# Kernel tuning notes

Hardware: AMD Instinct MI355X
Metric: run time of the kernel (lower is better)

## Reference

```python
import jax, jax.numpy as jnp
import numpy as np

N = 100000   # nodes
E = 1600000  # edges
H = 8        # heads
D = 16       # per-head dim
HD = H * D   # 128 = hidden_dim * num_heads == input_dim
G = 128      # graphs in batch
OUT = 64     # output_dim
EPS = 1e-3   # BatchNorm eps
NEG_SLOPE = 0.2
THRESH = 0.5


def setup_inputs() -> dict:
    key = jax.random.key(0)
    ks = jax.random.split(key, 20)
    rn = lambda k, s: jax.random.normal(k, s, jnp.float32) * 0.1
    return {
        "h": jax.random.normal(ks[0], (N, HD), jnp.float32),
        "src": jax.random.randint(ks[1], (E,), 0, N),
        "dst": jax.random.randint(ks[2], (E,), 0, N),
        "graph_ids": jnp.sort(jax.random.randint(ks[3], (N,), 0, G)),
        # GAT layer 0 params
        "W0": rn(ks[4], (HD, HD)), "al0": rn(ks[5], (H, D)), "ar0": rn(ks[6], (H, D)), "b0": rn(ks[7], (HD,)),
        "g0": jnp.ones((HD,), jnp.float32), "be0": jnp.zeros((HD,), jnp.float32),
        # GAT layer 1 params
        "W1": rn(ks[8], (HD, HD)), "al1": rn(ks[9], (H, D)), "ar1": rn(ks[10], (H, D)), "b1": rn(ks[11], (HD,)),
        "g1": jnp.ones((HD,), jnp.float32), "be1": jnp.zeros((HD,), jnp.float32),
        # MaskLinear prediction head
        "pred_W": rn(ks[12], (OUT, HD)), "pred_b": rn(ks[13], (OUT,)),
        "mask_real": jax.random.uniform(ks[14], (OUT, HD), jnp.float32),
    }


def _gat(h, W, al, ar, b, src, dst):
    # DGL GATConv: fc -> per-node attn halves -> edge LeakyReLU -> segment softmax over dst -> scatter-add
    feat = (h @ W).reshape(N, H, D)                 # [N,H,D]
    el = jnp.sum(feat * al, axis=-1)                # [N,H]
    er = jnp.sum(feat * ar, axis=-1)                # [N,H]
    e = jax.nn.leaky_relu(el[src] + er[dst], NEG_SLOPE)  # [E,H]
    emax = jax.ops.segment_max(e, dst, num_segments=N)   # [N,H]
    ee = jnp.exp(e - emax[dst])
    denom = jax.ops.segment_sum(ee, dst, num_segments=N) # [N,H]
    a = ee / denom[dst]                             # [E,H]
    msg = a[:, :, None] * feat[src]                 # [E,H,D]
    out = jax.ops.segment_sum(msg, dst, num_segments=N)  # [N,H,D]
    return out.reshape(N, HD) + b


def _bn(x, g, be):
    mu = jnp.mean(x, axis=0)
    var = jnp.mean((x - mu) ** 2, axis=0)
    return (x - mu) * jax.lax.rsqrt(var + EPS) * g + be


def reference(h, src, dst, graph_ids, W0, al0, ar0, b0, g0, be0,
              W1, al1, ar1, b1, g1, be1, pred_W, pred_b, mask_real):
    # layer 0: GAT -> BN -> ReLU (no residual)
    h1 = jax.nn.relu(_bn(_gat(h, W0, al0, ar0, b0, src, dst), g0, be0))
    # layer 1: GAT -> BN -> ReLU + residual
    h2 = jax.nn.relu(_bn(_gat(h1, W1, al1, ar1, b1, src, dst), g1, be1)) + h1
    # SumPooling over graphs in the batch
    pooled = jax.ops.segment_sum(h2, graph_ids, num_segments=G)  # [G,HD]
    # MaskLinear with binarized mask (eval path, no dropout)
    mask = (mask_real > THRESH).astype(pooled.dtype)
    return pooled @ (pred_W * mask).T + pred_b  # [G,OUT]
```

## Files before the change

kernel.cpp:

```cpp
#include <hip/hip_runtime.h>
#include <cstdint>

#define N_NODES 100000
#define N_EDGES 1600000
#define H 8
#define D 16
#define HD 128
#define G_GRAPHS 128
#define OUT_DIM 64
#define EPS 1e-3f
#define NEG 0.2f
#define NBUCK 196
#define BSHIFT 9
#define BCAP 10240
#define MT 64
#define APAD 136
#define NTILES 1563
#define GEMM_GRID 512
#define BNP_ROWS 64
#define BNS_ROWS 128
#define WTROWS 144
#define SRCMASK 0x1FFFF

typedef __attribute__((ext_vector_type(8))) short bf16x8;
typedef __attribute__((ext_vector_type(4))) float f32x4;
typedef __attribute__((ext_vector_type(8))) unsigned short u16x8;

__device__ __forceinline__ unsigned short f2bf(float x) {
    unsigned u = __float_as_uint(x);
    unsigned r = (u + 0x7FFFu + ((u >> 16) & 1u)) >> 16;
    return (unsigned short)r;
}
__device__ __forceinline__ float plo(unsigned q) {
    return __uint_as_float(q << 16);
}
__device__ __forceinline__ float phi(unsigned q) {
    return __uint_as_float(q & 0xFFFF0000u);
}
__device__ __forceinline__ unsigned packbf(float a, float b) {
    return (unsigned)f2bf(a) | ((unsigned)f2bf(b) << 16);
}

__global__ void convert_wt(const float* __restrict__ W0, const float* __restrict__ W1,
                           const float* __restrict__ al0, const float* __restrict__ ar0,
                           const float* __restrict__ al1, const float* __restrict__ ar1,
                           unsigned short* __restrict__ Wt0, unsigned short* __restrict__ Wt1,
                           int* __restrict__ bucketCnt, float* __restrict__ pooled,
                           float* __restrict__ sums01) {
    int t = blockIdx.x * blockDim.x + threadIdx.x;
    if (t < NBUCK) bucketCnt[t] = 0;
    if (t < 512) sums01[t] = 0.f;
    for (int i = t; i < G_GRAPHS * HD; i += gridDim.x * blockDim.x) pooled[i] = 0.f;
    if (t < HD * HD) {
        int k = t >> 7, n = t & 127;
        Wt0[n * HD + k] = f2bf(W0[t]);
        Wt1[n * HD + k] = f2bf(W1[t]);
        return;
    }
    int u = t - HD * HD;
    if (u < HD * 16) {
        int k = u >> 4, j = u & 15;
        int h = j & 7;
        const float* a0 = (j < 8) ? al0 : ar0;
        const float* a1 = (j < 8) ? al1 : ar1;
        float s0 = 0.f, s1 = 0.f;
#pragma unroll
        for (int d = 0; d < 16; ++d) {
            s0 += W0[k * HD + h * 16 + d] * a0[h * 16 + d];
            s1 += W1[k * HD + h * 16 + d] * a1[h * 16 + d];
        }
        Wt0[(HD + j) * HD + k] = f2bf(s0);
        Wt1[(HD + j) * HD + k] = f2bf(s1);
    }
}

__global__ __launch_bounds__(256) void bucket_scatter(const int4* __restrict__ src4,
                                                      const int4* __restrict__ dst4,
                                                      int* __restrict__ bucketCnt,
                                                      int* __restrict__ pairs) {
    __shared__ int hist[NBUCK];
    __shared__ int cur[NBUCK];
    int t = threadIdx.x;
    if (t < NBUCK) hist[t] = 0;
    __syncthreads();
    int base4 = blockIdx.x * 1024;
    const int NE4 = N_EDGES / 4;
    int4 s[4], d[4];
    int valid[4];
#pragma unroll
    for (int k = 0; k < 4; ++k) {
        int i4 = base4 + t + k * 256;
        if (i4 < NE4) {
            s[k] = src4[i4];
            d[k] = dst4[i4];
            valid[k] = 1;
            atomicAdd(&hist[d[k].x >> BSHIFT], 1);
            atomicAdd(&hist[d[k].y >> BSHIFT], 1);
            atomicAdd(&hist[d[k].z >> BSHIFT], 1);
            atomicAdd(&hist[d[k].w >> BSHIFT], 1);
        } else {
            valid[k] = 0;
        }
    }
    __syncthreads();
    if (t < NBUCK) {
        int c = hist[t];
        cur[t] = (c > 0) ? atomicAdd(&bucketCnt[t], c) : 0;
    }
    __syncthreads();
#pragma unroll
    for (int k = 0; k < 4; ++k) {
        if (valid[k]) {
            int ss[4] = {s[k].x, s[k].y, s[k].z, s[k].w};
            int dd[4] = {d[k].x, d[k].y, d[k].z, d[k].w};
#pragma unroll
            for (int j = 0; j < 4; ++j) {
                int b = dd[j] >> BSHIFT;
                int slot = atomicAdd(&cur[b], 1);
                pairs[(size_t)b * BCAP + slot] = ((dd[j] & 511) << 17) | ss[j];
            }
        }
    }
}

__global__ __launch_bounds__(256) void bucket_finish(const int* __restrict__ bucketCnt,
                                                     const int* __restrict__ pairs,
                                                     int2* __restrict__ ninfo,
                                                     int* __restrict__ csr_src) {
    __shared__ int hist[512];
    __shared__ int loc[512];
    __shared__ int bufA[256], bufB[256];
    __shared__ int bbase_sh;
    int b = blockIdx.x, t = threadIdx.x;
    int mycnt = bucketCnt[b];
    int base0 = b << BSHIFT;

    bufA[t] = (t < NBUCK) ? bucketCnt[t] : 0;
    __syncthreads();
    {
        int* a = bufA; int* bb = bufB;
        for (int off = 1; off < 256; off <<= 1) {
            int val = a[t];
            if (t >= off) val += a[t - off];
            bb[t] = val;
            __syncthreads();
            int* c = a; a = bb; bb = c;
        }
        if (t == 0) bbase_sh = a[b] - mycnt;
    }
    hist[t] = 0;
    hist[t + 256] = 0;
    __syncthreads();
    {
        const int4* p4 = (const int4*)&pairs[(size_t)b * BCAP];
        int n4 = mycnt >> 2;
        for (int i = t; i < n4; i += 256) {
            int4 w = p4[i];
            atomicAdd(&hist[(unsigned)w.x >> 17], 1);
            atomicAdd(&hist[(unsigned)w.y >> 17], 1);
            atomicAdd(&hist[(unsigned)w.z >> 17], 1);
            atomicAdd(&hist[(unsigned)w.w >> 17], 1);
        }
        for (int i = (n4 << 2) + t; i < mycnt; i += 256)
            atomicAdd(&hist[(unsigned)pairs[(size_t)b * BCAP + i] >> 17], 1);
    }
    __syncthreads();
    int s0 = hist[2 * t], s1 = hist[2 * t + 1];
    int ps = s0 + s1;
    bufA[t] = ps;
    __syncthreads();
    int total_excl;
    {
        int* a = bufA; int* bb = bufB;
        for (int off = 1; off < 256; off <<= 1) {
            int val = a[t];
            if (t >= off) val += a[t - off];
            bb[t] = val;
            __syncthreads();
            int* c = a; a = bb; bb = c;
        }
        total_excl = a[t] - ps;
    }
    int bbase = bbase_sh;
    loc[2 * t] = total_excl;
    loc[2 * t + 1] = total_excl + s0;
    int n0 = base0 + 2 * t, n1 = base0 + 2 * t + 1;
    if (n0 < N_NODES) ninfo[n0] = make_int2(bbase + total_excl, s0);
    if (n1 < N_NODES) ninfo[n1] = make_int2(bbase + total_excl + s0, s1);
    __syncthreads();
    {
        const int4* p4 = (const int4*)&pairs[(size_t)b * BCAP];
        int n4 = mycnt >> 2;
        for (int i = t; i < n4; i += 256) {
            int4 w = p4[i];
            int ws[4] = {w.x, w.y, w.z, w.w};
#pragma unroll
            for (int j = 0; j < 4; ++j) {
                int dl = (unsigned)ws[j] >> 17;
                int r = atomicAdd(&loc[dl], 1);
                csr_src[bbase + r] = ws[j] & SRCMASK;
            }
        }
        for (int i = (n4 << 2) + t; i < mycnt; i += 256) {
            int w = pairs[(size_t)b * BCAP + i];
            int dl = (unsigned)w >> 17;
            int r = atomicAdd(&loc[dl], 1);
            csr_src[bbase + r] = w & SRCMASK;
        }
    }
}

template <int MODE>
__device__ __forceinline__ void stage_load(const void* __restrict__ Xv, int gr, int scol,
                                           int nrows, const float* scs, const float* shs,
                                           u16x8 o[4]) {
    if (gr < nrows) {
        if (MODE == 0) {
            const float* X = (const float*)Xv;
#pragma unroll
            for (int i = 0; i < 4; ++i) {
                float4 va = *(const float4*)&X[(size_t)gr * HD + scol + i * 8];
                float4 vb = *(const float4*)&X[(size_t)gr * HD + scol + i * 8 + 4];
                o[i][0] = f2bf(va.x); o[i][1] = f2bf(va.y);
                o[i][2] = f2bf(va.z); o[i][3] = f2bf(va.w);
                o[i][4] = f2bf(vb.x); o[i][5] = f2bf(vb.y);
                o[i][6] = f2bf(vb.z); o[i][7] = f2bf(vb.w);
            }
        } else {
            const unsigned* X32 = (const unsigned*)Xv;
#pragma unroll
            for (int i = 0; i < 4; ++i) {
                uint4 u = *(const uint4*)&X32[(size_t)gr * 64 + (scol >> 1) + i * 4];
                f32x4 sa = *(const f32x4*)&scs[scol + i * 8];
                f32x4 sb = *(const f32x4*)&scs[scol + i * 8 + 4];
                f32x4 ha = *(const f32x4*)&shs[scol + i * 8];
                f32x4 hb = *(const f32x4*)&shs[scol + i * 8 + 4];
                float z0 = fmaxf(plo(u.x) * sa.x + ha.x, 0.f);
                float z1 = fmaxf(phi(u.x) * sa.y + ha.y, 0.f);
                float z2 = fmaxf(plo(u.y) * sa.z + ha.z, 0.f);
                float z3 = fmaxf(phi(u.y) * sa.w + ha.w, 0.f);
                float z4 = fmaxf(plo(u.z) * sb.x + hb.x, 0.f);
                float z5 = fmaxf(phi(u.z) * sb.y + hb.y, 0.f);
                float z6 = fmaxf(plo(u.w) * sb.z + hb.z, 0.f);
                float z7 = fmaxf(phi(u.w) * sb.w + hb.w, 0.f);
                o[i][0] = f2bf(z0); o[i][1] = f2bf(z1);
                o[i][2] = f2bf(z2); o[i][3] = f2bf(z3);
                o[i][4] = f2bf(z4); o[i][5] = f2bf(z5);
                o[i][6] = f2bf(z6); o[i][7] = f2bf(z7);
            }
        }
    } else {
#pragma unroll
        for (int i = 0; i < 4; ++i) o[i] = (u16x8)0;
    }
}

template <int MODE>
__global__ __launch_bounds__(256, 2) void gemm_mfma(const void* __restrict__ Xv,
                                                    const unsigned short* __restrict__ Wt,
                                                    unsigned short* __restrict__ Yb,
                                                    float* __restrict__ el,
                                                    float* __restrict__ er,
                                                    int nrows,
                                                    const float* __restrict__ sums,
                                                    const float* __restrict__ gam,
                                                    const float* __restrict__ bet) {
    __shared__ unsigned short As[2][MT * APAD];
    __shared__ __align__(16) float scs[HD];
    __shared__ __align__(16) float shs[HD];
    int tid = threadIdx.x;
    int wave = tid >> 6, lane = tid & 63;
    int qd = lane >> 4, l16 = lane & 15;

    if (MODE == 1) {
        if (tid < HD) {
            float invN = 1.0f / (float)N_NODES;
            float mu = sums[tid] * invN;
            float rs = rsqrtf(sums[HD + tid] * invN - mu * mu + EPS);
            float sc = rs * gam[tid];
            scs[tid] = sc;
            shs[tid] = bet[tid] - mu * sc;
        }
        __syncthreads();
    }

    bf16x8 bfr[9][4];
#pragma unroll
    for (int nt = 0; nt < 9; ++nt)
#pragma unroll
        for (int kb = 0; kb < 4; ++kb)
            bfr[nt][kb] = *(const bf16x8*)&Wt[(nt * 16 + l16) * HD + kb * 32 + qd * 8];

    int srow = tid >> 2, scol = (tid & 3) * 32;

    u16x8 o[4];
    int t = blockIdx.x;
    stage_load<MODE>(Xv, t * MT + srow, scol, nrows, scs, shs, o);
#pragma unroll
    for (int i = 0; i < 4; ++i)
        *(u16x8*)&As[0][srow * APAD + scol + i * 8] = o[i];
    __syncthreads();
    int cur = 0;

    for (; t < NTILES; t += gridDim.x) {
        int tn = t + (int)gridDim.x;
        bool more = tn < NTILES;
        if (more)
            stage_load<MODE>(Xv, tn * MT + srow, scol, nrows, scs, shs, o);
        f32x4 acc[9];
#pragma unroll
        for (int nt = 0; nt < 9; ++nt) acc[nt] = (f32x4){0.f, 0.f, 0.f, 0.f};
        bf16x8 afr[4];
#pragma unroll
        for (int kb = 0; kb < 4; ++kb)
            afr[kb] = *(const bf16x8*)&As[cur][(wave * 16 + l16) * APAD + kb * 32 + qd * 8];
#pragma unroll
        for (int nt = 0; nt < 9; ++nt)
#pragma unroll
            for (int kb = 0; kb < 4; ++kb)
                acc[nt] = __builtin_amdgcn_mfma_f32_16x16x32_bf16(afr[kb], bfr[nt][kb], acc[nt], 0, 0, 0);
        int orow = t * MT + wave * 16 + qd * 4;
        if (orow + 3 < nrows) {
#pragma unroll
            for (int nt = 0; nt < 8; ++nt)
#pragma unroll
                for (int r = 0; r < 4; ++r)
                    Yb[(size_t)(orow + r) * HD + nt * 16 + l16] = f2bf(acc[nt][r]);
#pragma unroll
            for (int r = 0; r < 4; ++r) {
                float v = acc[8][r];
                if (l16 < 8) el[(orow + r) * 8 + l16] = v;
                else er[(orow + r) * 8 + (l16 - 8)] = v;
            }
        } else {
#pragma unroll
            for (int nt = 0; nt < 8; ++nt)
                for (int r = 0; r < 4; ++r)
                    if (orow + r < nrows)
                        Yb[(size_t)(orow + r) * HD + nt * 16 + l16] = f2bf(acc[nt][r]);
            for (int r = 0; r < 4; ++r) {
                if (orow + r < nrows) {
                    float v = acc[8][r];
                    if (l16 < 8) el[(orow + r) * 8 + l16] = v;
                    else er[(orow + r) * 8 + (l16 - 8)] = v;
                }
            }
        }
        if (more) {
#pragma unroll
            for (int i = 0; i < 4; ++i)
                *(u16x8*)&As[cur ^ 1][srow * APAD + scol + i * 8] = o[i];
        }
        __syncthreads();
        cur ^= 1;
    }
}

__global__ __launch_bounds__(256) void gat_node(const int2* __restrict__ ninfo,
                                                const int* __restrict__ csr_src,
                                                const float* __restrict__ el,
                                                const float* __restrict__ er,
                                                const uint2* __restrict__ featq,
                                                unsigned* __restrict__ gatb) {
    int node = blockIdx.x * 4 + (threadIdx.x >> 6);
    if (node >= N_NODES) return;
    int lane = threadIdx.x & 63;
    int h7 = lane & 7;
    int eidx = lane >> 3;
    int l32 = lane & 31;
    int hacc = l32 >> 2;
    int half = lane >> 5;
    int ibase = half * 8 + hacc;

    int2 pd = ninfo[node];
    int p = pd.x;
    int cnt = pd.y;
    float ern = er[node * 8 + h7];
    float ds = 0.f, a0 = 0.f, a1 = 0.f, a2 = 0.f, a3 = 0.f;

    int nfull = cnt & ~7;
    if (nfull) {
        int s = csr_src[p + eidx];
        float x = el[(unsigned)s * 8u + h7];
        int c = 0;
        for (;;) {
            float v = x + ern;
            v = fmaxf(v, NEG * v);
            float e = __expf(v);
            ds += e;
            int cn = c + 8;
            int snext = 0; float xnext = 0.f;
            if (cn < nfull) {
                snext = csr_src[p + cn + eidx];
                xnext = el[(unsigned)snext * 8u + h7];
            }
#pragma unroll
            for (int k = 0; k < 4; ++k) {
                float ek = __shfl(e, ibase + 16 * k);
                int sk = __shfl(s, ibase + 16 * k);
                uint2 q = featq[(size_t)((unsigned)sk * 32u + (unsigned)l32)];
                a0 += ek * plo(q.x); a1 += ek * phi(q.x);
                a2 += ek * plo(q.y); a3 += ek * phi(q.y);
            }
            if (cn >= nfull) break;
            c = cn; s = snext; x = xnext;
        }
    }
    int rem = cnt & 7;
    if (rem) {
        int s = 0; float e = 0.f;
        if (eidx < rem) {
            s = csr_src[p + nfull + eidx];
            float v = el[(unsigned)s * 8u + h7] + ern;
            v = fmaxf(v, NEG * v);
            e = __expf(v);
        }
        ds += e;
        int nst = (rem + 1) >> 1;
        for (int k = 0; k < nst; ++k) {
            float ek = __shfl(e, ibase + 16 * k);
            int sk = __shfl(s, ibase + 16 * k);
            uint2 q = featq[(size_t)((unsigned)sk * 32u + (unsigned)l32)];
            a0 += ek * plo(q.x); a1 += ek * phi(q.x);
            a2 += ek * plo(q.y); a3 += ek * phi(q.y);
        }
    }
    ds += __shfl_xor(ds, 8);
    ds += __shfl_xor(ds, 16);
    ds += __shfl_xor(ds, 32);
    float dfull = __shfl(ds, hacc);
    float invd = dfull > 0.f ? 1.f / dfull : 0.f;
    a0 += __shfl_xor(a0, 32);
    a1 += __shfl_xor(a1, 32);
    a2 += __shfl_xor(a2, 32);
    a3 += __shfl_xor(a3, 32);
    if (half == 0) {
        uint2 w;
        w.x = packbf(a0 * invd, a1 * invd);
        w.y = packbf(a2 * invd, a3 * invd);
        ((uint2*)gatb)[(size_t)node * 32 + l32] = w;
    }
}

__global__ __launch_bounds__(256) void bn_stats(const unsigned* __restrict__ xb,
                                                float* __restrict__ sums, int nrows) {
    int cp = threadIdx.x & 63;
    int rr = threadIdx.x >> 6;
    int r0 = blockIdx.x * BNS_ROWS;
    int rend = r0 + BNS_ROWS < nrows ? r0 + BNS_ROWS : nrows;
    float s0 = 0.f, q0 = 0.f, s1 = 0.f, q1 = 0.f;
    for (int r = r0 + rr; r < rend; r += 4) {
        unsigned u = xb[(size_t)r * 64 + cp];
        float a = plo(u), b = phi(u);
        s0 += a; q0 += a * a;
        s1 += b; q1 += b * b;
    }
    __shared__ float red[4][256];
    red[0][threadIdx.x] = s0;
    red[1][threadIdx.x] = q0;
    red[2][threadIdx.x] = s1;
    red[3][threadIdx.x] = q1;
    __syncthreads();
    if (rr == 0) {
        int c0 = cp * 2, c1 = c0 + 1;
        float ts0 = red[0][cp] + red[0][cp + 64] + red[0][cp + 128] + red[0][cp + 192];
        float tq0 = red[1][cp] + red[1][cp + 64] + red[1][cp + 128] + red[1][cp + 192];
        float ts1 = red[2][cp] + red[2][cp + 64] + red[2][cp + 128] + red[2][cp + 192];
        float tq1 = red[3][cp] + red[3][cp + 64] + red[3][cp + 128] + red[3][cp + 192];
        atomicAdd(&sums[c0], ts0);
        atomicAdd(&sums[128 + c0], tq0);
        atomicAdd(&sums[c1], ts1);
        atomicAdd(&sums[128 + c1], tq1);
    }
}

__global__ __launch_bounds__(256) void bn_pool(const unsigned* __restrict__ gat1,
                                               const float* __restrict__ sums1,
                                               const float* __restrict__ g1v,
                                               const float* __restrict__ be1v,
                                               const unsigned* __restrict__ gat0,
                                               const float* __restrict__ sums0,
                                               const float* __restrict__ g0v,
                                               const float* __restrict__ be0v,
                                               const int* __restrict__ gid,
                                               float* __restrict__ pooled) {
    int cp = threadIdx.x & 63;
    int rr = threadIdx.x >> 6;
    int c0 = cp * 2, c1 = c0 + 1;
    float invN = 1.0f / (float)N_NODES;
    float mu10 = sums1[c0] * invN, mu11 = sums1[c1] * invN;
    float rs10 = rsqrtf(sums1[128 + c0] * invN - mu10 * mu10 + EPS);
    float rs11 = rsqrtf(sums1[128 + c1] * invN - mu11 * mu11 + EPS);
    float A10 = rs10 * g1v[c0], B10 = be1v[c0] - mu10 * A10;
    float A11 = rs11 * g1v[c1], B11 = be1v[c1] - mu11 * A11;
    float mu00 = sums0[c0] * invN, mu01 = sums0[c1] * invN;
    float rs00 = rsqrtf(sums0[128 + c0] * invN - mu00 * mu00 + EPS);
    float rs01 = rsqrtf(sums0[128 + c1] * invN - mu01 * mu01 + EPS);
    float A00 = rs00 * g0v[c0], B00 = be0v[c0] - mu00 * A00;
    float A01 = rs01 * g0v[c1], B01 = be0v[c1] - mu01 * A01;
    int r0 = blockIdx.x * BNP_ROWS;
    int rend = r0 + BNP_ROWS < N_NODES ? r0 + BNP_ROWS : N_NODES;
    int r = r0 + rr;
    if (r >= rend) return;
    float a0 = 0.f, a1 = 0.f;
    int cur = gid[r];
    for (; r < rend; r += 4) {
        int gg = gid[r];
        if (gg != cur) {
            atomicAdd(&pooled[cur * HD + c0], a0);
            atomicAdd(&pooled[cur * HD + c1], a1);
            a0 = a1 = 0.f;
            cur = gg;
        }
        unsigned u = gat1[(size_t)r * 64 + cp];
        float z0 = plo(u) * A10 + B10;
        float z1 = phi(u) * A11 + B11;
        z0 = z0 > 0.f ? z0 : 0.f;
        z1 = z1 > 0.f ? z1 : 0.f;
        unsigned v = gat0[(size_t)r * 64 + cp];
        float h0 = plo(v) * A00 + B00;
        float h1 = phi(v) * A01 + B01;
        h0 = h0 > 0.f ? h0 : 0.f;
        h1 = h1 > 0.f ? h1 : 0.f;
        a0 += z0 + h0;
        a1 += z1 + h1;
    }
    atomicAdd(&pooled[cur * HD + c0], a0);
    atomicAdd(&pooled[cur * HD + c1], a1);
}

__global__ void pred_kernel(const float* __restrict__ pooled, const float* __restrict__ W,
                            const float* __restrict__ b, const float* __restrict__ mask,
                            float* __restrict__ out) {
    int t = blockIdx.x * blockDim.x + threadIdx.x;
    if (t >= G_GRAPHS * OUT_DIM) return;
    int g = t >> 6, o = t & 63;
    float acc = b[o];
#pragma unroll 4
    for (int c = 0; c < HD; ++c) {
        float m = mask[o * HD + c] > 0.5f ? 1.f : 0.f;
        acc += pooled[g * HD + c] * W[o * HD + c] * m;
    }
    out[t] = acc;
}

extern "C" void kernel_launch(void* const* d_in, const int* in_sizes, int n_in,
                              void* d_out, int out_size, void* d_ws, size_t ws_size,
                              hipStream_t stream) {
    const float* h   = (const float*)d_in[0];
    const int*   src = (const int*)d_in[1];
    const int*   dst = (const int*)d_in[2];
    const int*   gid = (const int*)d_in[3];
    const float* W0  = (const float*)d_in[4];
    const float* al0 = (const float*)d_in[5];
    const float* ar0 = (const float*)d_in[6];
    const float* g0  = (const float*)d_in[8];
    const float* be0 = (const float*)d_in[9];
    const float* W1  = (const float*)d_in[10];
    const float* al1 = (const float*)d_in[11];
    const float* ar1 = (const float*)d_in[12];
    const float* g1  = (const float*)d_in[14];
    const float* be1 = (const float*)d_in[15];
    const float* pW  = (const float*)d_in[16];
    const float* pb  = (const float*)d_in[17];
    const float* msk = (const float*)d_in[18];
    float* out = (float*)d_out;

    unsigned short* gat0  = (unsigned short*)d_ws;
    unsigned short* gat1  = gat0 + (size_t)N_NODES * HD;
    unsigned short* featb = gat1 + (size_t)N_NODES * HD;
    float* el   = (float*)(featb + (size_t)N_NODES * HD);
    float* er   = el + (size_t)N_NODES * H;
    int2*  ninfo = (int2*)(er + (size_t)N_NODES * H);
    int*   csr_src = (int*)(ninfo + N_NODES);
    int*   bucketCnt = csr_src + N_EDGES;
    float* sums0  = (float*)(bucketCnt + 256);
    float* sums1  = sums0 + 256;
    float* pooled = sums1 + 256;
    unsigned short* wt0 = (unsigned short*)(pooled + G_GRAPHS * HD);
    unsigned short* wt1 = wt0 + WTROWS * HD;
    int*   pairs  = (int*)gat1;

    const int TB = 256;
    dim3 blk(TB);
    int bsc_blocks  = (N_EDGES + 4095) / 4096;
    int node_blocks = (N_NODES + 3) / 4;
    int bns_blocks  = (N_NODES + BNS_ROWS - 1) / BNS_ROWS;
    int bnp_blocks  = (N_NODES + BNP_ROWS - 1) / BNP_ROWS;
    int cw_blocks   = (HD * HD + HD * 16 + TB - 1) / TB;

    convert_wt<<<cw_blocks, blk, 0, stream>>>(W0, W1, al0, ar0, al1, ar1, wt0, wt1,
                                              bucketCnt, pooled, sums0);
    bucket_scatter<<<bsc_blocks, blk, 0, stream>>>((const int4*)src, (const int4*)dst,
                                                   bucketCnt, pairs);
    bucket_finish<<<NBUCK, blk, 0, stream>>>(bucketCnt, pairs, ninfo, csr_src);

    gemm_mfma<0><<<GEMM_GRID, blk, 0, stream>>>(h, wt0, featb, el, er, N_NODES,
                                                nullptr, nullptr, nullptr);
    gat_node<<<node_blocks, blk, 0, stream>>>(ninfo, csr_src, el, er,
                                              (const uint2*)featb, (unsigned*)gat0);
    bn_stats<<<bns_blocks, blk, 0, stream>>>((const unsigned*)gat0, sums0, N_NODES);

    gemm_mfma<1><<<GEMM_GRID, blk, 0, stream>>>(gat0, wt1, featb, el, er, N_NODES,
                                                sums0, g0, be0);
    gat_node<<<node_blocks, blk, 0, stream>>>(ninfo, csr_src, el, er,
                                              (const uint2*)featb, (unsigned*)gat1);
    bn_stats<<<bns_blocks, blk, 0, stream>>>((const unsigned*)gat1, sums1, N_NODES);
    bn_pool<<<bnp_blocks, blk, 0, stream>>>((const unsigned*)gat1, sums1, g1, be1,
                                            (const unsigned*)gat0, sums0, g0, be0,
                                            gid, pooled);

    pred_kernel<<<(G_GRAPHS * OUT_DIM + TB - 1) / TB, blk, 0, stream>>>(pooled, pW, pb, msk, out);
}
```

Before: 466.3 us.

## Store projected node features as FP8 and gather 8 channels per lane

The GEMM now packs projected features into FP8 (e4m3 via cvt_pk_fp8) instead of bf16, with the weight columns permuted so that each lane's 8 output channels form one contiguous 8-byte word. The GAT aggregation gathers 8-byte FP8 rows, two edges per lane group per step, and unpacks them with cvt_pk_f32_fp8, halving the bytes of the random neighbour-feature gather. It also skips loads for zero-weight tail edges. The cost is reduced precision of the messages, which may exceed the tolerance, and changed shuffle and reduction patterns.

Result: faster. 430.3 us (-7.7%).

```diff
diff --git a/kernel.cpp b/kernel.cpp
--- a/kernel.cpp
+++ b/kernel.cpp
@@ -41,6 +41,17 @@
     return (unsigned)f2bf(a) | ((unsigned)f2bf(b) << 16);
 }
 
+#define ACC8(qq, ee) do { \
+    auto f0_ = __builtin_amdgcn_cvt_pk_f32_fp8((qq).x, false); \
+    a[0] += (ee) * f0_[0]; a[1] += (ee) * f0_[1]; \
+    auto f1_ = __builtin_amdgcn_cvt_pk_f32_fp8((qq).x, true); \
+    a[2] += (ee) * f1_[0]; a[3] += (ee) * f1_[1]; \
+    auto f2_ = __builtin_amdgcn_cvt_pk_f32_fp8((qq).y, false); \
+    a[4] += (ee) * f2_[0]; a[5] += (ee) * f2_[1]; \
+    auto f3_ = __builtin_amdgcn_cvt_pk_f32_fp8((qq).y, true); \
+    a[6] += (ee) * f3_[0]; a[7] += (ee) * f3_[1]; \
+} while (0)
+
 __global__ void convert_wt(const float* __restrict__ W0, const float* __restrict__ W1,
                            const float* __restrict__ al0, const float* __restrict__ ar0,
                            const float* __restrict__ al1, const float* __restrict__ ar1,
@@ -53,8 +64,9 @@
     for (int i = t; i < G_GRAPHS * HD; i += gridDim.x * blockDim.x) pooled[i] = 0.f;
     if (t < HD * HD) {
         int k = t >> 7, n = t & 127;
-        Wt0[n * HD + k] = f2bf(W0[t]);
-        Wt1[n * HD + k] = f2bf(W1[t]);
+        int f = ((n & 15) << 3) | (n >> 4);
+        Wt0[n * HD + k] = f2bf(W0[k * HD + f]);
+        Wt1[n * HD + k] = f2bf(W1[k * HD + f]);
         return;
     }
     int u = t - HD * HD;
@@ -258,7 +270,7 @@
 template <int MODE>
 __global__ __launch_bounds__(256, 2) void gemm_mfma(const void* __restrict__ Xv,
                                                     const unsigned short* __restrict__ Wt,
-                                                    unsigned short* __restrict__ Yb,
+                                                    uint2* __restrict__ Y8,
                                                     float* __restrict__ el,
                                                     float* __restrict__ er,
                                                     int nrows,
@@ -322,10 +334,14 @@
         int orow = t * MT + wave * 16 + qd * 4;
         if (orow + 3 < nrows) {
 #pragma unroll
-            for (int nt = 0; nt < 8; ++nt)
-#pragma unroll
-                for (int r = 0; r < 4; ++r)
-                    Yb[(size_t)(orow + r) * HD + nt * 16 + l16] = f2bf(acc[nt][r]);
+            for (int r = 0; r < 4; ++r) {
+                unsigned lo = 0, hi = 0;
+                lo = __builtin_amdgcn_cvt_pk_fp8_f32(acc[0][r], acc[1][r], lo, false);
+                lo = __builtin_amdgcn_cvt_pk_fp8_f32(acc[2][r], acc[3][r], lo, true);
+                hi = __builtin_amdgcn_cvt_pk_fp8_f32(acc[4][r], acc[5][r], hi, false);
+                hi = __builtin_amdgcn_cvt_pk_fp8_f32(acc[6][r], acc[7][r], hi, true);
+                Y8[(size_t)(orow + r) * 16 + l16] = make_uint2(lo, hi);
+            }
 #pragma unroll
             for (int r = 0; r < 4; ++r) {
                 float v = acc[8][r];
@@ -333,13 +349,14 @@
                 else er[(orow + r) * 8 + (l16 - 8)] = v;
             }
         } else {
-#pragma unroll
-            for (int nt = 0; nt < 8; ++nt)
-                for (int r = 0; r < 4; ++r)
-                    if (orow + r < nrows)
-                        Yb[(size_t)(orow + r) * HD + nt * 16 + l16] = f2bf(acc[nt][r]);
             for (int r = 0; r < 4; ++r) {
                 if (orow + r < nrows) {
+                    unsigned lo = 0, hi = 0;
+                    lo = __builtin_amdgcn_cvt_pk_fp8_f32(acc[0][r], acc[1][r], lo, false);
+                    lo = __builtin_amdgcn_cvt_pk_fp8_f32(acc[2][r], acc[3][r], lo, true);
+                    hi = __builtin_amdgcn_cvt_pk_fp8_f32(acc[4][r], acc[5][r], hi, false);
+                    hi = __builtin_amdgcn_cvt_pk_fp8_f32(acc[6][r], acc[7][r], hi, true);
+                    Y8[(size_t)(orow + r) * 16 + l16] = make_uint2(lo, hi);
                     float v = acc[8][r];
                     if (l16 < 8) el[(orow + r) * 8 + l16] = v;
                     else er[(orow + r) * 8 + (l16 - 8)] = v;
@@ -360,23 +377,27 @@
                                                 const int* __restrict__ csr_src,
                                                 const float* __restrict__ el,
                                                 const float* __restrict__ er,
-                                                const uint2* __restrict__ featq,
+                                                const uint2* __restrict__ feat8q,
                                                 unsigned* __restrict__ gatb) {
     int node = blockIdx.x * 4 + (threadIdx.x >> 6);
     if (node >= N_NODES) return;
     int lane = threadIdx.x & 63;
     int h7 = lane & 7;
     int eidx = lane >> 3;
-    int l32 = lane & 31;
-    int hacc = l32 >> 2;
-    int half = lane >> 5;
-    int ibase = half * 8 + hacc;
+    int l16 = lane & 15;
+    int sub = lane >> 4;
+    int hacc8 = l16 >> 1;
+    int sl0 = sub * 8 + hacc8;
+    int sl1 = sl0 + 32;
 
     int2 pd = ninfo[node];
     int p = pd.x;
     int cnt = pd.y;
     float ern = er[node * 8 + h7];
-    float ds = 0.f, a0 = 0.f, a1 = 0.f, a2 = 0.f, a3 = 0.f;
+    float ds = 0.f;
+    float a[8];
+#pragma unroll
+    for (int i = 0; i < 8; ++i) a[i] = 0.f;
 
     int nfull = cnt & ~7;
     if (nfull) {
@@ -394,14 +415,12 @@
                 snext = csr_src[p + cn + eidx];
                 xnext = el[(unsigned)snext * 8u + h7];
             }
-#pragma unroll
-            for (int k = 0; k < 4; ++k) {
-                float ek = __shfl(e, ibase + 16 * k);
-                int sk = __shfl(s, ibase + 16 * k);
-                uint2 q = featq[(size_t)((unsigned)sk * 32u + (unsigned)l32)];
-                a0 += ek * plo(q.x); a1 += ek * phi(q.x);
-                a2 += ek * plo(q.y); a3 += ek * phi(q.y);
-            }
+            float e0 = __shfl(e, sl0); int s0 = __shfl(s, sl0);
+            float e1 = __shfl(e, sl1); int s1 = __shfl(s, sl1);
+            uint2 q0 = feat8q[(size_t)((unsigned)s0 * 16u + (unsigned)l16)];
+            uint2 q1 = feat8q[(size_t)((unsigned)s1 * 16u + (unsigned)l16)];
+            ACC8(q0, e0);
+            ACC8(q1, e1);
             if (cn >= nfull) break;
             c = cn; s = snext; x = xnext;
         }
@@ -416,29 +435,34 @@
             e = __expf(v);
         }
         ds += e;
-        int nst = (rem + 1) >> 1;
-        for (int k = 0; k < nst; ++k) {
-            float ek = __shfl(e, ibase + 16 * k);
-            int sk = __shfl(s, ibase + 16 * k);
-            uint2 q = featq[(size_t)((unsigned)sk * 32u + (unsigned)l32)];
-            a0 += ek * plo(q.x); a1 += ek * phi(q.x);
-            a2 += ek * plo(q.y); a3 += ek * phi(q.y);
+        float e0 = __shfl(e, sl0); int s0 = __shfl(s, sl0);
+        float e1 = __shfl(e, sl1); int s1 = __shfl(s, sl1);
+        if (e0 != 0.f) {
+            uint2 q0 = feat8q[(size_t)((unsigned)s0 * 16u + (unsigned)l16)];
+            ACC8(q0, e0);
+        }
+        if (e1 != 0.f) {
+            uint2 q1 = feat8q[(size_t)((unsigned)s1 * 16u + (unsigned)l16)];
+            ACC8(q1, e1);
         }
     }
     ds += __shfl_xor(ds, 8);
     ds += __shfl_xor(ds, 16);
     ds += __shfl_xor(ds, 32);
-    float dfull = __shfl(ds, hacc);
+    float dfull = __shfl(ds, hacc8);
     float invd = dfull > 0.f ? 1.f / dfull : 0.f;
-    a0 += __shfl_xor(a0, 32);
-    a1 += __shfl_xor(a1, 32);
-    a2 += __shfl_xor(a2, 32);
-    a3 += __shfl_xor(a3, 32);
-    if (half == 0) {
-        uint2 w;
-        w.x = packbf(a0 * invd, a1 * invd);
-        w.y = packbf(a2 * invd, a3 * invd);
-        ((uint2*)gatb)[(size_t)node * 32 + l32] = w;
+#pragma unroll
+    for (int i = 0; i < 8; ++i) {
+        a[i] += __shfl_xor(a[i], 16);
+        a[i] += __shfl_xor(a[i], 32);
+    }
+    if (sub == 0) {
+        uint4 w;
+        w.x = packbf(a[0] * invd, a[1] * invd);
+        w.y = packbf(a[2] * invd, a[3] * invd);
+        w.z = packbf(a[4] * invd, a[5] * invd);
+        w.w = packbf(a[6] * invd, a[7] * invd);
+        ((uint4*)gatb)[(size_t)node * 16 + l16] = w;
     }
 }
 
@@ -568,8 +592,8 @@
 
     unsigned short* gat0  = (unsigned short*)d_ws;
     unsigned short* gat1  = gat0 + (size_t)N_NODES * HD;
-    unsigned short* featb = gat1 + (size_t)N_NODES * HD;
-    float* el   = (float*)(featb + (size_t)N_NODES * HD);
+    unsigned char*  feat8 = (unsigned char*)(gat1 + (size_t)N_NODES * HD);
+    float* el   = (float*)(feat8 + (size_t)N_NODES * HD);
     float* er   = el + (size_t)N_NODES * H;
     int2*  ninfo = (int2*)(er + (size_t)N_NODES * H);
     int*   csr_src = (int*)(ninfo + N_NODES);
@@ -595,16 +619,16 @@
                                                    bucketCnt, pairs);
     bucket_finish<<<NBUCK, blk, 0, stream>>>(bucketCnt, pairs, ninfo, csr_src);
 
-    gemm_mfma<0><<<GEMM_GRID, blk, 0, stream>>>(h, wt0, featb, el, er, N_NODES,
+    gemm_mfma<0><<<GEMM_GRID, blk, 0, stream>>>(h, wt0, (uint2*)feat8, el, er, N_NODES,
                                                 nullptr, nullptr, nullptr);
     gat_node<<<node_blocks, blk, 0, stream>>>(ninfo, csr_src, el, er,
-                                              (const uint2*)featb, (unsigned*)gat0);
+                                              (const uint2*)feat8, (unsigned*)gat0);
     bn_stats<<<bns_blocks, blk, 0, stream>>>((const unsigned*)gat0, sums0, N_NODES);
 
-    gemm_mfma<1><<<GEMM_GRID, blk, 0, stream>>>(gat0, wt1, featb, el, er, N_NODES,
+    gemm_mfma<1><<<GEMM_GRID, blk, 0, stream>>>(gat0, wt1, (uint2*)feat8, el, er, N_NODES,
                                                 sums0, g0, be0);
     gat_node<<<node_blocks, blk, 0, stream>>>(ninfo, csr_src, el, er,
-                                              (const uint2*)featb, (unsigned*)gat1);
+                                              (const uint2*)feat8, (unsigned*)gat1);
     bn_stats<<<bns_blocks, blk, 0, stream>>>((const unsigned*)gat1, sums1, N_NODES);
     bn_pool<<<bnp_blocks, blk, 0, stream>>>((const unsigned*)gat1, sums1, g1, be1,
                                             (const unsigned*)gat0, sums0, g0, be0,
```
